# Performance work log

Measured on AMD Instinct MI355X. Metric: run time of the kernel, lower is better.

Reference implementation:

```python
import jax, jax.numpy as jnp
import numpy as np

T = 0.07        # temperature (hardcoded in CCM)
BN_EPS = 1e-5   # torch BatchNorm1d default eps (eval mode, running stats)


def _l2norm(x):
    # torch F.normalize(dim=1): x / max(||x||, 1e-12)
    n = jnp.linalg.norm(x, axis=1, keepdims=True)
    return x / jnp.maximum(n, 1e-12)


def _attn(q, k):
    # cosine similarity scaled by 1/t and 1/sqrt(num_keys)
    scale = jnp.asarray(k.shape[0], q.dtype) ** 0.5
    return (_l2norm(q) @ _l2norm(k).T) / T / scale


def setup_inputs() -> dict:
    key = jax.random.key(0)
    ks = jax.random.split(key, 24)
    D, N, BS, C, H = 2048, 1024, 64, 65, 128
    f32 = jnp.float32
    def g(k, shape, scale=1.0):
        return jax.random.normal(k, shape, f32) * scale
    return {
        "all_f": g(ks[0], (BS, D)),
        "embedding": _l2norm(g(ks[1], (N, D))),  # memory queue (normalized at init)
        "all_y": jax.random.randint(ks[2], (BS,), 0, C),
        "head_w1": g(ks[3], (D, H), 1.0 / np.sqrt(D)),
        "head_b1": jnp.zeros((H,), f32),
        "head_g": jax.random.uniform(ks[4], (H,), f32) + 0.5,
        "head_beta": g(ks[5], (H,), 0.1),
        "head_rm": g(ks[6], (H,), 0.1),
        "head_rv": jax.random.uniform(ks[7], (H,), f32) + 0.5,
        "head_w2": g(ks[8], (H, H), 1.0 / np.sqrt(H)),
        "head_b2": jnp.zeros((H,), f32),
        "mix_w1": g(ks[9], (2 * H, H), 1.0 / np.sqrt(2 * H)),
        "mix_b1": jnp.zeros((H,), f32),
        "mix_g": jax.random.uniform(ks[10], (H,), f32) + 0.5,
        "mix_beta": g(ks[11], (H,), 0.1),
        "mix_rm": g(ks[12], (H,), 0.1),
        "mix_rv": jax.random.uniform(ks[13], (H,), f32) + 0.5,
        "mix_w2": g(ks[14], (H, D), 1.0 / np.sqrt(H)),
        "mix_b2": jnp.zeros((D,), f32),
        "clf_w": g(ks[15], (D, C), 1.0 / np.sqrt(D)),
        "clf_b": jnp.zeros((C,), f32),
    }


def reference(all_f, embedding, all_y,
              head_w1, head_b1, head_g, head_beta, head_rm, head_rv, head_w2, head_b2,
              mix_w1, mix_b1, mix_g, mix_beta, mix_rm, mix_rv, mix_w2, mix_b2,
              clf_w, clf_b):
    # CCM.causal(all_f, embedding, all_y): returns [bs, num_classes]
    H = head_b2.shape[0]
    # z|x attention over the memory queue
    z_x = jax.nn.softmax(_attn(all_f, embedding), axis=-1)          # [bs, N]

    def head(x):
        h = x @ head_w1 + head_b1
        h = (h - head_rm) * jax.lax.rsqrt(head_rv + BN_EPS) * head_g + head_beta
        return jax.nn.relu(h) @ head_w2 + head_b2                   # [., 128]

    hf = head(all_f)        # [bs, 128]
    hz = head(embedding)    # [N, 128]
    # mixer layer 1 on concat([hf, hz]) decomposed into two matmuls + broadcast add
    h1 = hf @ mix_w1[:H] + mix_b1                                   # [bs, 128]
    h1 = h1[:, None, :] + (hz @ mix_w1[H:])[None, :, :]             # [bs, N, 128]
    h1 = (h1 - mix_rm) * jax.lax.rsqrt(mix_rv + BN_EPS) * mix_g + mix_beta
    h1 = jax.nn.relu(h1)
    mixed = h1 @ mix_w2 + mix_b2                                    # [bs, N, D]
    y_zx = jax.nn.softmax(mixed @ clf_w + clf_b, axis=-1)           # [bs, N, C] = p(y|z,x)
    # p(x): self-attention row-sums, softmax over the batch (all_y given -> this branch)
    p_x = jax.nn.softmax(_attn(all_f, all_f).sum(axis=1), axis=0)   # [bs]
    sum_x = jnp.einsum('b,bnc->nc', p_x, y_zx)                      # [N, C]
    return z_x @ sum_x                                              # [bs, C]
```

## Files before the change

### kernel.cpp

```cpp
#include <hip/hip_runtime.h>
#include <hip/hip_bf16.h>
#include <math.h>

#define D   2048
#define NQ  1024
#define BSZ 64
#define NC  65
#define HD  128

#define OFF_SCALEH 0
#define OFF_CH     128
#define OFF_BZC    256
#define OFF_BAC    384
#define OFF_BVEC   512
#define OFF_PXP    640
#define OFF_WC     896
#define OFF_SP     145280
#define OFF_SUMX   669568
#define OFF_FNB    751488
#define OFF_AFB    817024
#define OFF_EMBB   882560
#define OFF_W1T    1931136
#define OFF_WZT    2062208
#define OFF_WAT    2070400
#define OFF_MW2B   2078592
#define OFF_CWT    2226048
#define OFF_H1P    2307968

typedef __attribute__((ext_vector_type(8))) short    bf16x8;
typedef __attribute__((ext_vector_type(4))) float    f32x4;
typedef __attribute__((ext_vector_type(8))) unsigned short u16x8;
typedef __attribute__((ext_vector_type(2))) unsigned short u16x2;

__device__ inline unsigned short f2b(float v) {
    __hip_bfloat16 h = __float2bfloat16(v);
    return __builtin_bit_cast(unsigned short, h);
}

__global__ void __launch_bounds__(256) k_prep(const float* __restrict__ all_f,
                                              const float* __restrict__ emb,
                                              const float* __restrict__ head_w1,
                                              const float* __restrict__ head_b1,
                                              const float* __restrict__ head_g,
                                              const float* __restrict__ head_beta,
                                              const float* __restrict__ head_rm,
                                              const float* __restrict__ head_rv,
                                              const float* __restrict__ head_w2,
                                              const float* __restrict__ head_b2,
                                              const float* __restrict__ mix_w1,
                                              const float* __restrict__ mix_b1,
                                              const float* __restrict__ mix_g,
                                              const float* __restrict__ mix_beta,
                                              const float* __restrict__ mix_rm,
                                              const float* __restrict__ mix_rv,
                                              const float* __restrict__ mix_w2,
                                              const float* __restrict__ mix_b2,
                                              const float* __restrict__ clf_w,
                                              float* __restrict__ ws) {
    __shared__ float sbuf[128*66];
    int bid = blockIdx.x, t = threadIdx.x;
    if (bid == 0) {
        int h = t & 127, jq = t >> 7;
        float sb = 0.f, sa = 0.f;
        #pragma unroll 8
        for (int j = jq*64; j < jq*64 + 64; ++j) {
            float b2v = head_b2[j];
            sb = fmaf(b2v, mix_w1[(HD + j)*HD + h], sb);
            sa = fmaf(b2v, mix_w1[j*HD + h], sa);
        }
        sbuf[jq*256 + h]       = sb;
        sbuf[jq*256 + 128 + h] = sa;
        __syncthreads();
        if (jq == 0) {
            float s = head_g[h] * rsqrtf(head_rv[h] + 1e-5f);
            ws[OFF_SCALEH + h] = s;
            ws[OFF_CH + h] = (head_b1[h] - head_rm[h]) * s + head_beta[h];
            float ms = mix_g[h] * rsqrtf(mix_rv[h] + 1e-5f);
            float msh = mix_beta[h] - mix_rm[h] * ms;
            float sbT = sbuf[h] + sbuf[256 + h];
            float saT = sbuf[128 + h] + sbuf[256 + 128 + h];
            ws[OFF_BZC + h] = sbT * ms;
            ws[OFF_BAC + h] = fmaf(saT + mix_b1[h], ms, msh);
        }
    } else if (bid < 129) {
        int j = bid - 1;
        int h = t & 127, which = t >> 7;
        const float* M1 = mix_w1 + (which ? 0 : HD*HD);
        float ms = mix_g[h] * rsqrtf(mix_rv[h] + 1e-5f);
        float acc = 0.f;
        #pragma unroll 8
        for (int k = 0; k < HD; ++k)
            acc = fmaf(head_w2[j*HD + k], M1[k*HD + h], acc);
        unsigned short* dst = (unsigned short*)(ws + (which ? OFF_WAT : OFF_WZT));
        dst[h*HD + j] = f2b(acc * ms);
    } else if (bid < 165) {
        int r0 = (bid - 129) * 4;
        unsigned short* dst = (unsigned short*)(ws + OFF_MW2B);
        int i0 = t * 8;
        for (int rr = 0; rr < 4; ++rr) {
            int r = r0 + rr;
            u16x8 o;
            if (r < HD || r == HD) {
                const float* src = (r < HD) ? (mix_w2 + (size_t)r * D) : mix_b2;
                float4 f1 = *(const float4*)(src + i0);
                float4 f2 = *(const float4*)(src + i0 + 4);
                o[0]=f2b(f1.x); o[1]=f2b(f1.y); o[2]=f2b(f1.z); o[3]=f2b(f1.w);
                o[4]=f2b(f2.x); o[5]=f2b(f2.y); o[6]=f2b(f2.z); o[7]=f2b(f2.w);
            } else {
                o[0]=0;o[1]=0;o[2]=0;o[3]=0;o[4]=0;o[5]=0;o[6]=0;o[7]=0;
            }
            *(u16x8*)(dst + (size_t)r*D + i0) = o;
        }
    } else if (bid < 181) {
        int k0 = (bid - 165) * 128;
        float (*tile)[66] = (float(*)[66])sbuf;
        for (int i = t; i < 128*65; i += 256) {
            int r = i / 65;
            tile[r][i - 65*r] = clf_w[(size_t)k0*65 + i];
        }
        __syncthreads();
        unsigned short* cwt = (unsigned short*)(ws + OFF_CWT);
        for (int idx = t; idx < 80*16; idx += 256) {
            int c = idx >> 4, kq = idx & 15;
            u16x8 v;
            #pragma unroll
            for (int j = 0; j < 8; ++j)
                v[j] = (c < NC) ? f2b(tile[kq*8 + j][c]) : (unsigned short)0;
            *(u16x8*)(cwt + (size_t)c*D + k0 + kq*8) = v;
        }
    } else if (bid < 245) {
        int b = bid - 181;
        const float* src = all_f + (size_t)b * D;
        int i0 = t * 8;
        float4 f1 = *(const float4*)(src + i0);
        float4 f2 = *(const float4*)(src + i0 + 4);
        float s = f1.x*f1.x + f1.y*f1.y + f1.z*f1.z + f1.w*f1.w
                + f2.x*f2.x + f2.y*f2.y + f2.z*f2.z + f2.w*f2.w;
        s += __shfl_xor(s, 1);  s += __shfl_xor(s, 2);  s += __shfl_xor(s, 4);
        s += __shfl_xor(s, 8);  s += __shfl_xor(s, 16); s += __shfl_xor(s, 32);
        if ((t & 63) == 0) sbuf[t >> 6] = s;
        __syncthreads();
        float tot = sbuf[0] + sbuf[1] + sbuf[2] + sbuf[3];
        float rn = 1.f / fmaxf(sqrtf(tot), 1e-12f);
        unsigned short* fnb = (unsigned short*)(ws + OFF_FNB) + (size_t)b * D;
        unsigned short* afb = (unsigned short*)(ws + OFF_AFB) + (size_t)b * D;
        u16x8 on, oa;
        on[0]=f2b(f1.x*rn); on[1]=f2b(f1.y*rn); on[2]=f2b(f1.z*rn); on[3]=f2b(f1.w*rn);
        on[4]=f2b(f2.x*rn); on[5]=f2b(f2.y*rn); on[6]=f2b(f2.z*rn); on[7]=f2b(f2.w*rn);
        oa[0]=f2b(f1.x); oa[1]=f2b(f1.y); oa[2]=f2b(f1.z); oa[3]=f2b(f1.w);
        oa[4]=f2b(f2.x); oa[5]=f2b(f2.y); oa[6]=f2b(f2.z); oa[7]=f2b(f2.w);
        *(u16x8*)(fnb + i0) = on;
        *(u16x8*)(afb + i0) = oa;
    } else if (bid < 757) {
        int n0 = (bid - 245) * 2;
        unsigned short* dst = (unsigned short*)(ws + OFF_EMBB);
        int i0 = t * 8;
        for (int r = 0; r < 2; ++r) {
            const float* src = emb + (size_t)(n0 + r) * D;
            float4 f1 = *(const float4*)(src + i0);
            float4 f2 = *(const float4*)(src + i0 + 4);
            u16x8 o;
            o[0]=f2b(f1.x); o[1]=f2b(f1.y); o[2]=f2b(f1.z); o[3]=f2b(f1.w);
            o[4]=f2b(f2.x); o[5]=f2b(f2.y); o[6]=f2b(f2.z); o[7]=f2b(f2.w);
            *(u16x8*)(dst + (size_t)(n0 + r)*D + i0) = o;
        }
    } else {
        int rb = bid - 757;
        float (*tile)[33] = (float(*)[33])sbuf;
        int k0 = (rb >> 2) * 128, h0 = (rb & 3) * 32;
        int hh = t & 31, kk = t >> 5;
        for (int r = 0; r < 16; ++r)
            tile[kk + r*8][hh] = head_w1[(size_t)(k0 + kk + r*8)*HD + h0 + hh];
        __syncthreads();
        unsigned short* dst = (unsigned short*)(ws + OFF_W1T);
        int kcol = (t & 63) * 2, hrow = t >> 6;
        for (int r = 0; r < 8; ++r) {
            int h = hrow + r*4;
            u16x2 v;
            v[0] = f2b(tile[kcol][h]);
            v[1] = f2b(tile[kcol + 1][h]);
            *(u16x2*)(dst + (size_t)(h0 + h)*D + k0 + kcol) = v;
        }
    }
}

__global__ void __launch_bounds__(512) k_main(const float* __restrict__ clf_b,
                                              float* __restrict__ ws) {
    __shared__ float part[2][32][128];
    __shared__ float wcp[8][16][16];
    int bid = blockIdx.x, t = threadIdx.x;
    int lane = t & 63, wv = t >> 6;
    int row16 = lane & 15, kgrp = lane >> 4;
    if (bid < 128) {
        const unsigned short* fnb  = (const unsigned short*)(ws + OFF_FNB);
        const unsigned short* embb = (const unsigned short*)(ws + OFF_EMBB);
        int nt = bid & 15, ks = bid >> 4;
        int b0 = (wv & 3) * 16;
        int n0 = nt*64 + (wv >> 2) * 32;
        const unsigned short* Ap = fnb  + (size_t)(b0 + row16)*D + ks*256 + kgrp*8;
        const unsigned short* B0 = embb + (size_t)(n0 + row16)*D + ks*256 + kgrp*8;
        const unsigned short* B1 = B0 + 16*D;
        f32x4 a0 = {0,0,0,0}, a1 = {0,0,0,0};
        #pragma unroll
        for (int s = 0; s < 8; ++s) {
            bf16x8 a = *(const bf16x8*)(Ap + s*32);
            a0 = __builtin_amdgcn_mfma_f32_16x16x32_bf16(a, *(const bf16x8*)(B0 + s*32), a0, 0, 0, 0);
            a1 = __builtin_amdgcn_mfma_f32_16x16x32_bf16(a, *(const bf16x8*)(B1 + s*32), a1, 0, 0, 0);
        }
        float* Sp = ws + OFF_SP + (size_t)ks * BSZ * NQ;
        #pragma unroll
        for (int r = 0; r < 4; ++r) {
            float* rowp = Sp + (size_t)(b0 + kgrp*4 + r)*NQ + n0;
            rowp[row16]      = a0[r];
            rowp[16 + row16] = a1[r];
        }
    } else if (bid < 196) {
        int role = bid - 128;
        int tile = role >> 1, kh = role & 1;
        bool isF = tile >= 32;
        const unsigned short* Arow = isF
            ? (const unsigned short*)(ws + OFF_AFB) + (size_t)(tile - 32) * 32 * D
            : (const unsigned short*)(ws + OFF_EMBB) + (size_t)tile * 32 * D;
        const unsigned short* w1t = (const unsigned short*)(ws + OFF_W1T);
        int hgrp = wv & 3, kq = wv >> 2;
        int koff = kh*1024 + kq*512;
        const unsigned short* Ap = Arow + (size_t)row16*D + koff + kgrp*8;
        const unsigned short* B0 = w1t + (size_t)(hgrp*32 + row16)*D + koff + kgrp*8;
        const unsigned short* B1 = B0 + 16*D;
        f32x4 h00 = {0,0,0,0}, h01 = {0,0,0,0}, h10 = {0,0,0,0}, h11 = {0,0,0,0};
        #pragma unroll 4
        for (int s = 0; s < 16; ++s) {
            bf16x8 a0 = *(const bf16x8*)(Ap + s*32);
            bf16x8 a1 = *(const bf16x8*)(Ap + 16*D + s*32);
            bf16x8 b0 = *(const bf16x8*)(B0 + s*32);
            bf16x8 b1 = *(const bf16x8*)(B1 + s*32);
            h00 = __builtin_amdgcn_mfma_f32_16x16x32_bf16(a0, b0, h00, 0, 0, 0);
            h01 = __builtin_amdgcn_mfma_f32_16x16x32_bf16(a0, b1, h01, 0, 0, 0);
            h10 = __builtin_amdgcn_mfma_f32_16x16x32_bf16(a1, b0, h10, 0, 0, 0);
            h11 = __builtin_amdgcn_mfma_f32_16x16x32_bf16(a1, b1, h11, 0, 0, 0);
        }
        int mb = kgrp*4, hc0 = hgrp*32 + row16, hc1 = hc0 + 16;
        #pragma unroll
        for (int r = 0; r < 4; ++r) {
            part[kq][mb + r][hc0]      = h00[r];
            part[kq][mb + r][hc1]      = h01[r];
            part[kq][16 + mb + r][hc0] = h10[r];
            part[kq][16 + mb + r][hc1] = h11[r];
        }
        __syncthreads();
        int row = t >> 4, c8 = (t & 15) * 8;
        float* dst = ws + OFF_H1P + (size_t)kh*1088*HD + (size_t)(tile*32 + row)*HD + c8;
        float4 o0, o1;
        o0.x = part[0][row][c8+0] + part[1][row][c8+0];
        o0.y = part[0][row][c8+1] + part[1][row][c8+1];
        o0.z = part[0][row][c8+2] + part[1][row][c8+2];
        o0.w = part[0][row][c8+3] + part[1][row][c8+3];
        o1.x = part[0][row][c8+4] + part[1][row][c8+4];
        o1.y = part[0][row][c8+5] + part[1][row][c8+5];
        o1.z = part[0][row][c8+6] + part[1][row][c8+6];
        o1.w = part[0][row][c8+7] + part[1][row][c8+7];
        *(float4*)dst = o0;
        *(float4*)(dst + 4) = o1;
    } else if (bid < 241) {
        int w = bid - 196;
        int mt = w / 5, ntile = w % 5;
        const unsigned short* mw2b = (const unsigned short*)(ws + OFF_MW2B);
        const unsigned short* cwt  = (const unsigned short*)(ws + OFF_CWT);
        const unsigned short* Ap = mw2b + (size_t)(mt*16 + row16)*D + wv*256 + kgrp*8;
        const unsigned short* Bp = cwt  + (size_t)(ntile*16 + row16)*D + wv*256 + kgrp*8;
        f32x4 acc = {0,0,0,0};
        #pragma unroll
        for (int s = 0; s < 8; ++s)
            acc = __builtin_amdgcn_mfma_f32_16x16x32_bf16(
                *(const bf16x8*)(Ap + s*32), *(const bf16x8*)(Bp + s*32), acc, 0, 0, 0);
        #pragma unroll
        for (int r = 0; r < 4; ++r)
            wcp[wv][kgrp*4 + r][row16] = acc[r];
        __syncthreads();
        if (t < 256) {
            int j = t >> 4, c16 = t & 15;
            float s = 0.f;
            #pragma unroll
            for (int q = 0; q < 8; ++q) s += wcp[q][j][c16];
            int jj = mt*16 + j, c = ntile*16 + c16;
            unsigned short* wct = (unsigned short*)(ws + OFF_WC);
            if (jj < HD)       wct[(size_t)c*HD + jj] = f2b(s);
            else if (jj == HD) ws[OFF_BVEC + c] = (c < NC) ? s + clf_b[c] : -1e30f;
        }
    } else {
        int pb = bid - 241;
        const unsigned short* fnb = (const unsigned short*)(ws + OFF_FNB);
        int bq = wv & 3, kq = (wv >> 2) + pb*2;
        int b0 = bq*16;
        const unsigned short* Ap = fnb + (size_t)(b0 + row16)*D + kq*512 + kgrp*8;
        const unsigned short* Bp = fnb + (size_t)row16*D + kq*512 + kgrp*8;
        f32x4 acc[4];
        #pragma unroll
        for (int nt = 0; nt < 4; ++nt) acc[nt] = (f32x4){0.f,0.f,0.f,0.f};
        #pragma unroll 2
        for (int s = 0; s < 16; ++s) {
            bf16x8 a = *(const bf16x8*)(Ap + s*32);
            #pragma unroll
            for (int nt = 0; nt < 4; ++nt)
                acc[nt] = __builtin_amdgcn_mfma_f32_16x16x32_bf16(
                    a, *(const bf16x8*)(Bp + (size_t)nt*16*D + s*32), acc[nt], 0, 0, 0);
        }
        #pragma unroll
        for (int r = 0; r < 4; ++r) {
            float v = acc[0][r] + acc[1][r] + acc[2][r] + acc[3][r];
            v += __shfl_xor(v, 1); v += __shfl_xor(v, 2);
            v += __shfl_xor(v, 4); v += __shfl_xor(v, 8);
            if (row16 == 0)
                ws[OFF_PXP + kq*64 + b0 + kgrp*4 + r] = v;
        }
    }
}

__global__ void __launch_bounds__(512) k_mixfin(const float* __restrict__ ws,
                                                float* __restrict__ wsw) {
    __shared__ unsigned short wcs[80][136];
    __shared__ unsigned short ush[32][136];
    __shared__ float a2s[64][132];
    __shared__ float b2s[32][132];
    __shared__ float redp[8][80];
    __shared__ float sumxs[2][80];
    int bid = blockIdx.x, t = threadIdx.x;
    int lane = t & 63, wv = t >> 6;
    int row16 = lane & 15, kgrp = lane >> 4;

    const unsigned short* wct = (const unsigned short*)(ws + OFF_WC);
    for (int i = t; i < 80*16; i += 512) {
        int r = i >> 4, cc = (i & 15) * 8;
        *(u16x8*)&wcs[r][cc] = *(const u16x8*)(wct + (size_t)r*HD + cc);
    }

    int frow = t >> 4, fc8 = (t & 15) * 8;
    int rt = wv >> 2, wv2 = wv & 3;
    int hcA = wv2*32 + row16, hcB = hcA + 16;
    int mb = kgrp*4;
    #pragma unroll
    for (int ft = 0; ft < 3; ++ft) {
        int tile = (ft == 0) ? (bid >> 3) : (31 + ft);
        bool isF = (ft != 0);
        const float* h0p = ws + OFF_H1P + (size_t)(tile*32 + frow)*HD + fc8;
        const float* h1p = h0p + (size_t)1088*HD;
        if (ft) __syncthreads();
        #pragma unroll
        for (int j = 0; j < 8; ++j) {
            int col = fc8 + j;
            float v = h0p[j] + h1p[j];
            ush[frow][col] = f2b(fmaxf(fmaf(v, ws[OFF_SCALEH + col], ws[OFF_CH + col]), 0.f));
        }
        __syncthreads();
        const unsigned short* wt = (const unsigned short*)(ws + (isF ? OFF_WAT : OFF_WZT));
        const unsigned short* W0 = wt + (size_t)(wv2*32 + row16)*HD + kgrp*8;
        const unsigned short* W1b = W0 + 16*HD;
        f32x4 o0 = {0,0,0,0}, o1 = {0,0,0,0};
        #pragma unroll
        for (int s = 0; s < 4; ++s) {
            bf16x8 a = *(const bf16x8*)(&ush[rt*16 + row16][s*32 + kgrp*8]);
            o0 = __builtin_amdgcn_mfma_f32_16x16x32_bf16(a, *(const bf16x8*)(W0 + s*32), o0, 0, 0, 0);
            o1 = __builtin_amdgcn_mfma_f32_16x16x32_bf16(a, *(const bf16x8*)(W1b + s*32), o1, 0, 0, 0);
        }
        int boff = isF ? OFF_BAC : OFF_BZC;
        float bz0 = ws[boff + hcA], bz1 = ws[boff + hcB];
        #pragma unroll
        for (int r = 0; r < 4; ++r) {
            int orow = rt*16 + mb + r;
            if (ft == 0) {
                b2s[orow][hcA] = o0[r] + bz0;
                b2s[orow][hcB] = o1[r] + bz1;
            } else {
                a2s[(ft-1)*32 + orow][hcA] = o0[r] + bz0;
                a2s[(ft-1)*32 + orow][hcB] = o1[r] + bz1;
            }
        }
    }

    const float invTS = 1.0f / (0.07f * 8.0f);
    float sv = (ws[OFF_PXP + lane] + ws[OFF_PXP + 64 + lane]
              + ws[OFF_PXP + 128 + lane] + ws[OFF_PXP + 192 + lane]) * invTS;
    float m2 = sv;
    m2 = fmaxf(m2, __shfl_xor(m2, 1));  m2 = fmaxf(m2, __shfl_xor(m2, 2));
    m2 = fmaxf(m2, __shfl_xor(m2, 4));  m2 = fmaxf(m2, __shfl_xor(m2, 8));
    m2 = fmaxf(m2, __shfl_xor(m2, 16)); m2 = fmaxf(m2, __shfl_xor(m2, 32));
    float e2 = __expf(sv - m2);
    float ssum = e2;
    ssum += __shfl_xor(ssum, 1);  ssum += __shfl_xor(ssum, 2);  ssum += __shfl_xor(ssum, 4);
    ssum += __shfl_xor(ssum, 8);  ssum += __shfl_xor(ssum, 16); ssum += __shfl_xor(ssum, 32);
    float px = e2 / ssum;
    float bvl[5];
    #pragma unroll
    for (int ct = 0; ct < 5; ++ct) bvl[ct] = ws[OFF_BVEC + ct*16 + row16];
    __syncthreads();

    int bt = wv & 3, ng = wv >> 2;
    float4 a2lo[4], a2hi[4];
    #pragma unroll
    for (int kt = 0; kt < 4; ++kt) {
        a2lo[kt] = *(const float4*)(&a2s[bt*16 + row16][kt*32 + kgrp*8]);
        a2hi[kt] = *(const float4*)(&a2s[bt*16 + row16][kt*32 + kgrp*8 + 4]);
    }
    int r0 = (bid & 7) * 4;
    #pragma unroll
    for (int pass = 0; pass < 2; ++pass) {
        const float* b2r = &b2s[r0 + pass*2 + ng][0];
        bf16x8 af[4];
        #pragma unroll
        for (int kt = 0; kt < 4; ++kt) {
            float4 blo = *(const float4*)(b2r + kt*32 + kgrp*8);
            float4 bhi = *(const float4*)(b2r + kt*32 + kgrp*8 + 4);
            bf16x8 v;
            v[0] = (short)f2b(fmaxf(a2lo[kt].x + blo.x, 0.f));
            v[1] = (short)f2b(fmaxf(a2lo[kt].y + blo.y, 0.f));
            v[2] = (short)f2b(fmaxf(a2lo[kt].z + blo.z, 0.f));
            v[3] = (short)f2b(fmaxf(a2lo[kt].w + blo.w, 0.f));
            v[4] = (short)f2b(fmaxf(a2hi[kt].x + bhi.x, 0.f));
            v[5] = (short)f2b(fmaxf(a2hi[kt].y + bhi.y, 0.f));
            v[6] = (short)f2b(fmaxf(a2hi[kt].z + bhi.z, 0.f));
            v[7] = (short)f2b(fmaxf(a2hi[kt].w + bhi.w, 0.f));
            af[kt] = v;
        }
        f32x4 acc[5];
        #pragma unroll
        for (int ct = 0; ct < 5; ++ct) acc[ct] = (f32x4){0.f,0.f,0.f,0.f};
        #pragma unroll
        for (int ct = 0; ct < 5; ++ct)
            #pragma unroll
            for (int kt = 0; kt < 4; ++kt)
                acc[ct] = __builtin_amdgcn_mfma_f32_16x16x32_bf16(
                    af[kt], *(const bf16x8*)(&wcs[ct*16 + row16][kt*32 + kgrp*8]),
                    acc[ct], 0, 0, 0);
        float outp[5] = {0.f, 0.f, 0.f, 0.f, 0.f};
        #pragma unroll
        for (int r = 0; r < 4; ++r) {
            float v0 = acc[0][r] + bvl[0];
            float v1 = acc[1][r] + bvl[1];
            float v2 = acc[2][r] + bvl[2];
            float v3 = acc[3][r] + bvl[3];
            float v4 = acc[4][r] + bvl[4];
            float m = fmaxf(fmaxf(fmaxf(v0, v1), fmaxf(v2, v3)), v4);
            m = fmaxf(m, __shfl_xor(m, 1)); m = fmaxf(m, __shfl_xor(m, 2));
            m = fmaxf(m, __shfl_xor(m, 4)); m = fmaxf(m, __shfl_xor(m, 8));
            float e0 = __expf(v0 - m), e1 = __expf(v1 - m), e2v = __expf(v2 - m);
            float e3 = __expf(v3 - m), e4 = __expf(v4 - m);
            float s = e0 + e1 + e2v + e3 + e4;
            s += __shfl_xor(s, 1); s += __shfl_xor(s, 2);
            s += __shfl_xor(s, 4); s += __shfl_xor(s, 8);
            float pxr = __shfl(px, bt*16 + kgrp*4 + r);
            float scale = pxr / s;
            outp[0] = fmaf(e0, scale, outp[0]);
            outp[1] = fmaf(e1, scale, outp[1]);
            outp[2] = fmaf(e2v, scale, outp[2]);
            outp[3] = fmaf(e3, scale, outp[3]);
            outp[4] = fmaf(e4, scale, outp[4]);
        }
        #pragma unroll
        for (int ct = 0; ct < 5; ++ct) {
            float v = outp[ct];
            v += __shfl_xor(v, 16); v += __shfl_xor(v, 32);
            outp[ct] = v;
        }
        if (kgrp == 0) {
            #pragma unroll
            for (int ct = 0; ct < 5; ++ct) redp[wv][ct*16 + row16] = outp[ct];
        }
        __syncthreads();
        if (t < 160) {
            int half = (t >= 80) ? 1 : 0;
            int c = t - 80*half;
            int nn = bid*4 + pass*2 + half;
            wsw[OFF_SUMX + (size_t)nn*80 + c] =
                redp[half*4 + 0][c] + redp[half*4 + 1][c]
              + redp[half*4 + 2][c] + redp[half*4 + 3][c];
        }
        __syncthreads();
    }
}

__global__ void __launch_bounds__(512) k_outz(const float* __restrict__ ws, float* __restrict__ out) {
    __shared__ float red8m[8], red8s[8];
    __shared__ float zrow[NQ];
    __shared__ float parts[8][128];
    int b = blockIdx.x, t = threadIdx.x;
    int lane = t & 63, wvv = t >> 6;
    const float invTS = 1.0f / (0.07f * 32.0f);
    const float* Sp = ws + OFF_SP + (size_t)b * NQ;
    float v0, v1;
    {
        float s = 0.f;
        #pragma unroll
        for (int p = 0; p < 8; ++p) s += Sp[(size_t)p*BSZ*NQ + t];
        v0 = s * invTS;
        s = 0.f;
        #pragma unroll
        for (int p = 0; p < 8; ++p) s += Sp[(size_t)p*BSZ*NQ + 512 + t];
        v1 = s * invTS;
    }
    float vmax = fmaxf(v0, v1);
    vmax = fmaxf(vmax, __shfl_xor(vmax, 1));  vmax = fmaxf(vmax, __shfl_xor(vmax, 2));
    vmax = fmaxf(vmax, __shfl_xor(vmax, 4));  vmax = fmaxf(vmax, __shfl_xor(vmax, 8));
    vmax = fmaxf(vmax, __shfl_xor(vmax, 16)); vmax = fmaxf(vmax, __shfl_xor(vmax, 32));
    if (lane == 0) red8m[wvv] = vmax;
    __syncthreads();
    float m = red8m[0];
    #pragma unroll
    for (int q = 1; q < 8; ++q) m = fmaxf(m, red8m[q]);
    float e0 = __expf(v0 - m), e1 = __expf(v1 - m);
    float ss = e0 + e1;
    ss += __shfl_xor(ss, 1);  ss += __shfl_xor(ss, 2);  ss += __shfl_xor(ss, 4);
    ss += __shfl_xor(ss, 8);  ss += __shfl_xor(ss, 16); ss += __shfl_xor(ss, 32);
    if (lane == 0) red8s[wvv] = ss;
    __syncthreads();
    float S = red8s[0] + red8s[1] + red8s[2] + red8s[3]
            + red8s[4] + red8s[5] + red8s[6] + red8s[7];
    float inv = 1.f / S;
    zrow[t]       = e0 * inv;
    zrow[512 + t] = e1 * inv;
    __syncthreads();
    const float* Sx = ws + OFF_SUMX;
    int c2 = 64 + (lane & 15);
    int nbase = wvv * 128;
    float a0 = 0.f, a1 = 0.f;
    #pragma unroll 8
    for (int k = 0; k < 128; ++k) {
        float z = zrow[nbase + k];
        const float* srow = Sx + (size_t)(nbase + k) * 80;
        a0 = fmaf(z, srow[lane], a0);
        a1 = fmaf(z, srow[c2], a1);
    }
    parts[wvv][lane] = a0;
    if (lane < 16) parts[wvv][64 + lane] = a1;
    __syncthreads();
    if (t < NC) {
        float s = 0.f;
        #pragma unroll
        for (int q = 0; q < 8; ++q) s += parts[q][t];
        out[b*NC + t] = s;
    }
}

extern "C" void kernel_launch(void* const* d_in, const int* in_sizes, int n_in,
                              void* d_out, int out_size, void* d_ws, size_t ws_size,
                              hipStream_t stream) {
    const float* all_f    = (const float*)d_in[0];
    const float* emb      = (const float*)d_in[1];
    const float* head_w1  = (const float*)d_in[3];
    const float* head_b1  = (const float*)d_in[4];
    const float* head_g   = (const float*)d_in[5];
    const float* head_beta= (const float*)d_in[6];
    const float* head_rm  = (const float*)d_in[7];
    const float* head_rv  = (const float*)d_in[8];
    const float* head_w2  = (const float*)d_in[9];
    const float* head_b2  = (const float*)d_in[10];
    const float* mix_w1   = (const float*)d_in[11];
    const float* mix_b1   = (const float*)d_in[12];
    const float* mix_g    = (const float*)d_in[13];
    const float* mix_beta = (const float*)d_in[14];
    const float* mix_rm   = (const float*)d_in[15];
    const float* mix_rv   = (const float*)d_in[16];
    const float* mix_w2   = (const float*)d_in[17];
    const float* mix_b2   = (const float*)d_in[18];
    const float* clf_w    = (const float*)d_in[19];
    const float* clf_b    = (const float*)d_in[20];
    float* ws  = (float*)d_ws;
    float* out = (float*)d_out;

    hipLaunchKernelGGL(k_prep, dim3(821), dim3(256), 0, stream,
                       all_f, emb, head_w1, head_b1, head_g, head_beta, head_rm, head_rv,
                       head_w2, head_b2, mix_w1, mix_b1, mix_g, mix_beta, mix_rm, mix_rv,
                       mix_w2, mix_b2, clf_w, ws);
    hipLaunchKernelGGL(k_main,   dim3(243), dim3(512), 0, stream, clf_b, ws);
    hipLaunchKernelGGL(k_mixfin, dim3(256), dim3(512), 0, stream, ws, ws);
    hipLaunchKernelGGL(k_outz,   dim3(64),  dim3(512), 0, stream, ws, out);
}
```

Before: 60.34 us.

## Double mixfin grid, batch head matmuls, store LDS in bf16, split outz by class

k_mixfin now launches twice as many blocks, each handling one pass instead of two. The three per-tile head matmuls are merged behind a single barrier, and intermediate a2/b2 tiles are stored in LDS as bf16 to shrink shared memory and raise occupancy. k_outz is split four ways across class chunks for more blocks, and its softmax max-subtraction is dropped. This removes barriers and underutilization on small grids, at the cost of redundant loads of shared inputs, extra bf16 rounding, and softmax overflow safety that now relies on bounded inputs.

```diff
diff --git a/kernel.cpp b/kernel.cpp
--- a/kernel.cpp
+++ b/kernel.cpp
@@ -35,6 +35,9 @@
 __device__ inline unsigned short f2b(float v) {
     __hip_bfloat16 h = __float2bfloat16(v);
     return __builtin_bit_cast(unsigned short, h);
+}
+__device__ inline float bf2f(unsigned short u) {
+    return __builtin_bit_cast(float, ((unsigned)u) << 16);
 }
 
 __global__ void __launch_bounds__(256) k_prep(const float* __restrict__ all_f,
@@ -316,14 +319,13 @@
     }
 }
 
-__global__ void __launch_bounds__(512) k_mixfin(const float* __restrict__ ws,
-                                                float* __restrict__ wsw) {
+__global__ void __launch_bounds__(512, 4) k_mixfin(const float* __restrict__ ws,
+                                                   float* __restrict__ wsw) {
     __shared__ unsigned short wcs[80][136];
-    __shared__ unsigned short ush[32][136];
-    __shared__ float a2s[64][132];
-    __shared__ float b2s[32][132];
+    __shared__ unsigned short ushA[96][136];
+    __shared__ unsigned short a2s[64][136];
+    __shared__ unsigned short b2s[32][136];
     __shared__ float redp[8][80];
-    __shared__ float sumxs[2][80];
     int bid = blockIdx.x, t = threadIdx.x;
     int lane = t & 63, wv = t >> 6;
     int row16 = lane & 15, kgrp = lane >> 4;
@@ -334,46 +336,19 @@
         *(u16x8*)&wcs[r][cc] = *(const u16x8*)(wct + (size_t)r*HD + cc);
     }
 
+    int tb = bid >> 4;
     int frow = t >> 4, fc8 = (t & 15) * 8;
-    int rt = wv >> 2, wv2 = wv & 3;
-    int hcA = wv2*32 + row16, hcB = hcA + 16;
-    int mb = kgrp*4;
-    #pragma unroll
-    for (int ft = 0; ft < 3; ++ft) {
-        int tile = (ft == 0) ? (bid >> 3) : (31 + ft);
-        bool isF = (ft != 0);
-        const float* h0p = ws + OFF_H1P + (size_t)(tile*32 + frow)*HD + fc8;
+    #pragma unroll
+    for (int g = 0; g < 3; ++g) {
+        int u = frow + g*32;
+        int h1row = (u < 32) ? (tb*32 + u) : (1024 + (u - 32));
+        const float* h0p = ws + OFF_H1P + (size_t)h1row*HD + fc8;
         const float* h1p = h0p + (size_t)1088*HD;
-        if (ft) __syncthreads();
         #pragma unroll
         for (int j = 0; j < 8; ++j) {
             int col = fc8 + j;
             float v = h0p[j] + h1p[j];
-            ush[frow][col] = f2b(fmaxf(fmaf(v, ws[OFF_SCALEH + col], ws[OFF_CH + col]), 0.f));
-        }
-        __syncthreads();
-        const unsigned short* wt = (const unsigned short*)(ws + (isF ? OFF_WAT : OFF_WZT));
-        const unsigned short* W0 = wt + (size_t)(wv2*32 + row16)*HD + kgrp*8;
-        const unsigned short* W1b = W0 + 16*HD;
-        f32x4 o0 = {0,0,0,0}, o1 = {0,0,0,0};
-        #pragma unroll
-        for (int s = 0; s < 4; ++s) {
-            bf16x8 a = *(const bf16x8*)(&ush[rt*16 + row16][s*32 + kgrp*8]);
-            o0 = __builtin_amdgcn_mfma_f32_16x16x32_bf16(a, *(const bf16x8*)(W0 + s*32), o0, 0, 0, 0);
-            o1 = __builtin_amdgcn_mfma_f32_16x16x32_bf16(a, *(const bf16x8*)(W1b + s*32), o1, 0, 0, 0);
-        }
-        int boff = isF ? OFF_BAC : OFF_BZC;
-        float bz0 = ws[boff + hcA], bz1 = ws[boff + hcB];
-        #pragma unroll
-        for (int r = 0; r < 4; ++r) {
-            int orow = rt*16 + mb + r;
-            if (ft == 0) {
-                b2s[orow][hcA] = o0[r] + bz0;
-                b2s[orow][hcB] = o1[r] + bz1;
-            } else {
-                a2s[(ft-1)*32 + orow][hcA] = o0[r] + bz0;
-                a2s[(ft-1)*32 + orow][hcB] = o1[r] + bz1;
-            }
+            ushA[u][col] = f2b(fmaxf(fmaf(v, ws[OFF_SCALEH + col], ws[OFF_CH + col]), 0.f));
         }
     }
 
@@ -394,119 +369,125 @@
     for (int ct = 0; ct < 5; ++ct) bvl[ct] = ws[OFF_BVEC + ct*16 + row16];
     __syncthreads();
 
+    #pragma unroll
+    for (int i = 0; i < 3; ++i) {
+        int task = wv + i*8;
+        int rt6 = task >> 2, cg = task & 3;
+        bool isF = rt6 >= 2;
+        const unsigned short* wt = (const unsigned short*)(ws + (isF ? OFF_WAT : OFF_WZT));
+        const unsigned short* W0 = wt + (size_t)(cg*32 + row16)*HD + kgrp*8;
+        const unsigned short* W1b = W0 + 16*HD;
+        f32x4 o0 = {0,0,0,0}, o1 = {0,0,0,0};
+        #pragma unroll
+        for (int s = 0; s < 4; ++s) {
+            bf16x8 a = *(const bf16x8*)(&ushA[rt6*16 + row16][s*32 + kgrp*8]);
+            o0 = __builtin_amdgcn_mfma_f32_16x16x32_bf16(a, *(const bf16x8*)(W0 + s*32), o0, 0, 0, 0);
+            o1 = __builtin_amdgcn_mfma_f32_16x16x32_bf16(a, *(const bf16x8*)(W1b + s*32), o1, 0, 0, 0);
+        }
+        int hcA = cg*32 + row16, hcB = hcA + 16;
+        int boff = isF ? OFF_BAC : OFF_BZC;
+        float bz0 = ws[boff + hcA], bz1 = ws[boff + hcB];
+        #pragma unroll
+        for (int r = 0; r < 4; ++r) {
+            int orow = rt6*16 + kgrp*4 + r;
+            if (orow < 32) {
+                b2s[orow][hcA] = f2b(o0[r] + bz0);
+                b2s[orow][hcB] = f2b(o1[r] + bz1);
+            } else {
+                a2s[orow - 32][hcA] = f2b(o0[r] + bz0);
+                a2s[orow - 32][hcB] = f2b(o1[r] + bz1);
+            }
+        }
+    }
+    __syncthreads();
+
     int bt = wv & 3, ng = wv >> 2;
-    float4 a2lo[4], a2hi[4];
+    u16x8 a2f[4];
+    #pragma unroll
+    for (int kt = 0; kt < 4; ++kt)
+        a2f[kt] = *(const u16x8*)&a2s[bt*16 + row16][kt*32 + kgrp*8];
+    int b2row = (bid & 15)*2 + ng;
+    bf16x8 af[4];
     #pragma unroll
     for (int kt = 0; kt < 4; ++kt) {
-        a2lo[kt] = *(const float4*)(&a2s[bt*16 + row16][kt*32 + kgrp*8]);
-        a2hi[kt] = *(const float4*)(&a2s[bt*16 + row16][kt*32 + kgrp*8 + 4]);
-    }
-    int r0 = (bid & 7) * 4;
-    #pragma unroll
-    for (int pass = 0; pass < 2; ++pass) {
-        const float* b2r = &b2s[r0 + pass*2 + ng][0];
-        bf16x8 af[4];
-        #pragma unroll
-        for (int kt = 0; kt < 4; ++kt) {
-            float4 blo = *(const float4*)(b2r + kt*32 + kgrp*8);
-            float4 bhi = *(const float4*)(b2r + kt*32 + kgrp*8 + 4);
-            bf16x8 v;
-            v[0] = (short)f2b(fmaxf(a2lo[kt].x + blo.x, 0.f));
-            v[1] = (short)f2b(fmaxf(a2lo[kt].y + blo.y, 0.f));
-            v[2] = (short)f2b(fmaxf(a2lo[kt].z + blo.z, 0.f));
-            v[3] = (short)f2b(fmaxf(a2lo[kt].w + blo.w, 0.f));
-            v[4] = (short)f2b(fmaxf(a2hi[kt].x + bhi.x, 0.f));
-            v[5] = (short)f2b(fmaxf(a2hi[kt].y + bhi.y, 0.f));
-            v[6] = (short)f2b(fmaxf(a2hi[kt].z + bhi.z, 0.f));
-            v[7] = (short)f2b(fmaxf(a2hi[kt].w + bhi.w, 0.f));
-            af[kt] = v;
-        }
-        f32x4 acc[5];
-        #pragma unroll
-        for (int ct = 0; ct < 5; ++ct) acc[ct] = (f32x4){0.f,0.f,0.f,0.f};
-        #pragma unroll
-        for (int ct = 0; ct < 5; ++ct)
-            #pragma unroll
-            for (int kt = 0; kt < 4; ++kt)
-                acc[ct] = __builtin_amdgcn_mfma_f32_16x16x32_bf16(
-                    af[kt], *(const bf16x8*)(&wcs[ct*16 + row16][kt*32 + kgrp*8]),
-                    acc[ct], 0, 0, 0);
-        float outp[5] = {0.f, 0.f, 0.f, 0.f, 0.f};
-        #pragma unroll
-        for (int r = 0; r < 4; ++r) {
-            float v0 = acc[0][r] + bvl[0];
-            float v1 = acc[1][r] + bvl[1];
-            float v2 = acc[2][r] + bvl[2];
-            float v3 = acc[3][r] + bvl[3];
-            float v4 = acc[4][r] + bvl[4];
-            float m = fmaxf(fmaxf(fmaxf(v0, v1), fmaxf(v2, v3)), v4);
-            m = fmaxf(m, __shfl_xor(m, 1)); m = fmaxf(m, __shfl_xor(m, 2));
-            m = fmaxf(m, __shfl_xor(m, 4)); m = fmaxf(m, __shfl_xor(m, 8));
-            float e0 = __expf(v0 - m), e1 = __expf(v1 - m), e2v = __expf(v2 - m);
-            float e3 = __expf(v3 - m), e4 = __expf(v4 - m);
-            float s = e0 + e1 + e2v + e3 + e4;
-            s += __shfl_xor(s, 1); s += __shfl_xor(s, 2);
-            s += __shfl_xor(s, 4); s += __shfl_xor(s, 8);
-            float pxr = __shfl(px, bt*16 + kgrp*4 + r);
-            float scale = pxr / s;
-            outp[0] = fmaf(e0, scale, outp[0]);
-            outp[1] = fmaf(e1, scale, outp[1]);
-            outp[2] = fmaf(e2v, scale, outp[2]);
-            outp[3] = fmaf(e3, scale, outp[3]);
-            outp[4] = fmaf(e4, scale, outp[4]);
-        }
-        #pragma unroll
-        for (int ct = 0; ct < 5; ++ct) {
-            float v = outp[ct];
-            v += __shfl_xor(v, 16); v += __shfl_xor(v, 32);
-            outp[ct] = v;
-        }
-        if (kgrp == 0) {
-            #pragma unroll
-            for (int ct = 0; ct < 5; ++ct) redp[wv][ct*16 + row16] = outp[ct];
-        }
-        __syncthreads();
-        if (t < 160) {
-            int half = (t >= 80) ? 1 : 0;
-            int c = t - 80*half;
-            int nn = bid*4 + pass*2 + half;
-            wsw[OFF_SUMX + (size_t)nn*80 + c] =
-                redp[half*4 + 0][c] + redp[half*4 + 1][c]
-              + redp[half*4 + 2][c] + redp[half*4 + 3][c];
-        }
-        __syncthreads();
+        u16x8 bv = *(const u16x8*)&b2s[b2row][kt*32 + kgrp*8];
+        bf16x8 v;
+        #pragma unroll
+        for (int j = 0; j < 8; ++j)
+            v[j] = (short)f2b(fmaxf(bf2f(a2f[kt][j]) + bf2f(bv[j]), 0.f));
+        af[kt] = v;
+    }
+    f32x4 acc[5];
+    #pragma unroll
+    for (int ct = 0; ct < 5; ++ct) acc[ct] = (f32x4){0.f,0.f,0.f,0.f};
+    #pragma unroll
+    for (int ct = 0; ct < 5; ++ct)
+        #pragma unroll
+        for (int kt = 0; kt < 4; ++kt)
+            acc[ct] = __builtin_amdgcn_mfma_f32_16x16x32_bf16(
+                af[kt], *(const bf16x8*)(&wcs[ct*16 + row16][kt*32 + kgrp*8]),
+                acc[ct], 0, 0, 0);
+    float outp[5] = {0.f, 0.f, 0.f, 0.f, 0.f};
+    #pragma unroll
+    for (int r = 0; r < 4; ++r) {
+        float v0 = acc[0][r] + bvl[0];
+        float v1 = acc[1][r] + bvl[1];
+        float v2 = acc[2][r] + bvl[2];
+        float v3 = acc[3][r] + bvl[3];
+        float v4 = acc[4][r] + bvl[4];
+        float m = fmaxf(fmaxf(fmaxf(v0, v1), fmaxf(v2, v3)), v4);
+        m = fmaxf(m, __shfl_xor(m, 1)); m = fmaxf(m, __shfl_xor(m, 2));
+        m = fmaxf(m, __shfl_xor(m, 4)); m = fmaxf(m, __shfl_xor(m, 8));
+        float e0 = __expf(v0 - m), e1 = __expf(v1 - m), e2v = __expf(v2 - m);
+        float e3 = __expf(v3 - m), e4 = __expf(v4 - m);
+        float s = e0 + e1 + e2v + e3 + e4;
+        s += __shfl_xor(s, 1); s += __shfl_xor(s, 2);
+        s += __shfl_xor(s, 4); s += __shfl_xor(s, 8);
+        float pxr = __shfl(px, bt*16 + kgrp*4 + r);
+        float scale = pxr / s;
+        outp[0] = fmaf(e0, scale, outp[0]);
+        outp[1] = fmaf(e1, scale, outp[1]);
+        outp[2] = fmaf(e2v, scale, outp[2]);
+        outp[3] = fmaf(e3, scale, outp[3]);
+        outp[4] = fmaf(e4, scale, outp[4]);
+    }
+    #pragma unroll
+    for (int ct = 0; ct < 5; ++ct) {
+        float v = outp[ct];
+        v += __shfl_xor(v, 16); v += __shfl_xor(v, 32);
+        outp[ct] = v;
+    }
+    if (kgrp == 0) {
+        #pragma unroll
+        for (int ct = 0; ct < 5; ++ct) redp[wv][ct*16 + row16] = outp[ct];
+    }
+    __syncthreads();
+    if (t < 160) {
+        int half = (t >= 80) ? 1 : 0;
+        int c = t - 80*half;
+        int nn = bid*2 + half;
+        wsw[OFF_SUMX + (size_t)nn*80 + c] =
+            redp[half*4 + 0][c] + redp[half*4 + 1][c]
+          + redp[half*4 + 2][c] + redp[half*4 + 3][c];
     }
 }
 
 __global__ void __launch_bounds__(512) k_outz(const float* __restrict__ ws, float* __restrict__ out) {
-    __shared__ float red8m[8], red8s[8];
+    __shared__ float red8s[8];
     __shared__ float zrow[NQ];
-    __shared__ float parts[8][128];
-    int b = blockIdx.x, t = threadIdx.x;
+    __shared__ float parts[8][20];
+    int bid = blockIdx.x, t = threadIdx.x;
     int lane = t & 63, wvv = t >> 6;
+    int b = bid >> 2, cq = bid & 3;
     const float invTS = 1.0f / (0.07f * 32.0f);
     const float* Sp = ws + OFF_SP + (size_t)b * NQ;
-    float v0, v1;
-    {
-        float s = 0.f;
-        #pragma unroll
-        for (int p = 0; p < 8; ++p) s += Sp[(size_t)p*BSZ*NQ + t];
-        v0 = s * invTS;
-        s = 0.f;
-        #pragma unroll
-        for (int p = 0; p < 8; ++p) s += Sp[(size_t)p*BSZ*NQ + 512 + t];
-        v1 = s * invTS;
-    }
-    float vmax = fmaxf(v0, v1);
-    vmax = fmaxf(vmax, __shfl_xor(vmax, 1));  vmax = fmaxf(vmax, __shfl_xor(vmax, 2));
-    vmax = fmaxf(vmax, __shfl_xor(vmax, 4));  vmax = fmaxf(vmax, __shfl_xor(vmax, 8));
-    vmax = fmaxf(vmax, __shfl_xor(vmax, 16)); vmax = fmaxf(vmax, __shfl_xor(vmax, 32));
-    if (lane == 0) red8m[wvv] = vmax;
-    __syncthreads();
-    float m = red8m[0];
-    #pragma unroll
-    for (int q = 1; q < 8; ++q) m = fmaxf(m, red8m[q]);
-    float e0 = __expf(v0 - m), e1 = __expf(v1 - m);
+    float s0 = 0.f, s1 = 0.f;
+    #pragma unroll
+    for (int p = 0; p < 8; ++p) {
+        s0 += Sp[(size_t)p*BSZ*NQ + t];
+        s1 += Sp[(size_t)p*BSZ*NQ + 512 + t];
+    }
+    float e0 = __expf(s0 * invTS), e1 = __expf(s1 * invTS);
     float ss = e0 + e1;
     ss += __shfl_xor(ss, 1);  ss += __shfl_xor(ss, 2);  ss += __shfl_xor(ss, 4);
     ss += __shfl_xor(ss, 8);  ss += __shfl_xor(ss, 16); ss += __shfl_xor(ss, 32);
@@ -519,24 +500,24 @@
     zrow[512 + t] = e1 * inv;
     __syncthreads();
     const float* Sx = ws + OFF_SUMX;
-    int c2 = 64 + (lane & 15);
     int nbase = wvv * 128;
-    float a0 = 0.f, a1 = 0.f;
-    #pragma unroll 8
-    for (int k = 0; k < 128; ++k) {
-        float z = zrow[nbase + k];
-        const float* srow = Sx + (size_t)(nbase + k) * 80;
-        a0 = fmaf(z, srow[lane], a0);
-        a1 = fmaf(z, srow[c2], a1);
-    }
-    parts[wvv][lane] = a0;
-    if (lane < 16) parts[wvv][64 + lane] = a1;
+    if (lane < 20) {
+        int c = cq*20 + lane;
+        float a0 = 0.f;
+        #pragma unroll 8
+        for (int k = 0; k < 128; ++k)
+            a0 = fmaf(zrow[nbase + k], Sx[(size_t)(nbase + k)*80 + c], a0);
+        parts[wvv][lane] = a0;
+    }
     __syncthreads();
-    if (t < NC) {
-        float s = 0.f;
-        #pragma unroll
-        for (int q = 0; q < 8; ++q) s += parts[q][t];
-        out[b*NC + t] = s;
+    if (t < 20) {
+        int cg = cq*20 + t;
+        if (cg < NC) {
+            float s = 0.f;
+            #pragma unroll
+            for (int q = 0; q < 8; ++q) s += parts[q][t];
+            out[b*NC + cg] = s;
+        }
     }
 }
 
@@ -571,6 +552,6 @@
                        head_w2, head_b2, mix_w1, mix_b1, mix_g, mix_beta, mix_rm, mix_rv,
                        mix_w2, mix_b2, clf_w, ws);
     hipLaunchKernelGGL(k_main,   dim3(243), dim3(512), 0, stream, clf_b, ws);
-    hipLaunchKernelGGL(k_mixfin, dim3(256), dim3(512), 0, stream, ws, ws);
-    hipLaunchKernelGGL(k_outz,   dim3(64),  dim3(512), 0, stream, ws, out);
-}
+    hipLaunchKernelGGL(k_mixfin, dim3(512), dim3(512), 0, stream, ws, ws);
+    hipLaunchKernelGGL(k_outz,   dim3(256), dim3(512), 0, stream, ws, out);
+}
```

After: 59.37 us (median of 2 runs). No clear change (-1.6%).
